# Kernel optimization log

Measured on AMD Instinct MI355X. Metric: run time of the kernel, lower is better.

The kernel has to match this reference:

```python
import jax, jax.numpy as jnp
import numpy as np

N = 100_000      # nodes
E = 3_200_000    # edges (avg degree 32)
D = 128          # input_dim == hidden_dim
L = 3            # num_layers
G = 64           # number of graphs in the batch
EPS = 1e-5       # LayerNorm eps


def setup_inputs() -> dict:
    key = jax.random.key(0)
    ks = jax.random.split(key, 8)
    x = jax.random.normal(ks[0], (N, D), dtype=jnp.float32)
    edge_index = jax.random.randint(ks[1], (2, E), 0, N, dtype=jnp.int64)
    edge_weight = jax.random.normal(ks[2], (E,), dtype=jnp.float32)
    batch = jnp.sort(jax.random.randint(ks[3], (N,), 0, G, dtype=jnp.int64))
    s = 1.0 / np.sqrt(D)
    W_pos = jax.random.normal(ks[4], (L, D, D), dtype=jnp.float32) * s
    W_neg = jax.random.normal(ks[5], (L, D, D), dtype=jnp.float32) * s
    b_pos = jnp.zeros((L, D), dtype=jnp.float32)
    b_neg = jnp.zeros((L, D), dtype=jnp.float32)
    gamma = jnp.ones((D,), dtype=jnp.float32)
    beta = jnp.zeros((D,), dtype=jnp.float32)
    return dict(x=x, edge_index=edge_index, edge_weight=edge_weight, batch=batch,
                W_pos=W_pos, b_pos=b_pos, W_neg=W_neg, b_neg=b_neg,
                gamma=gamma, beta=beta)


def _branch_norm(src, dst, mask, n):
    # GCN symmetric normalization on the masked subgraph with unit edge weights
    # and self-loops (fill_value=1). deg counted on target nodes (PyG col).
    deg = 1.0 + jax.ops.segment_sum(mask, dst, num_segments=n)  # >= 1
    dinv_sqrt = jax.lax.rsqrt(deg)
    edge_norm = mask * dinv_sqrt[src] * dinv_sqrt[dst]          # 0 on masked-out edges
    self_norm = 1.0 / deg                                       # self-loop coefficient
    return edge_norm, self_norm


def _gcn_layer(h, W, b, src, dst, edge_norm, self_norm):
    h = h @ W  # [N, H], lin without bias (PyG GCNConv)
    agg = jax.ops.segment_sum(edge_norm[:, None] * h[src], dst,
                              num_segments=h.shape[0])
    return agg + h * self_norm[:, None] + b


def reference(x, edge_index, edge_weight, batch, W_pos, b_pos, W_neg, b_neg, gamma, beta):
    src, dst = edge_index[0], edge_index[1]
    pos_mask = (edge_weight > 0).astype(x.dtype)
    neg_mask = (edge_weight < 0).astype(x.dtype)
    n = x.shape[0]
    pos_en, pos_sn = _branch_norm(src, dst, pos_mask, n)
    neg_en, neg_sn = _branch_norm(src, dst, neg_mask, n)
    h = x
    for l in range(W_pos.shape[0]):
        hp = _gcn_layer(h, W_pos[l], b_pos[l], src, dst, pos_en, pos_sn)
        hn = _gcn_layer(h, W_neg[l], b_neg[l], src, dst, neg_en, neg_sn)
        h = jax.nn.relu(hp) - jax.nn.relu(hn)
    # global mean pool over graphs
    counts = jax.ops.segment_sum(jnp.ones((n,), h.dtype), batch, num_segments=G)
    sums = jax.ops.segment_sum(h, batch, num_segments=G)
    pooled = sums / jnp.clip(counts, 1.0)[:, None]  # [G, H]
    # LayerNorm
    mu = jnp.mean(pooled, axis=-1, keepdims=True)
    var = jnp.mean(jnp.square(pooled - mu), axis=-1, keepdims=True)
    return (pooled - mu) * jax.lax.rsqrt(var + EPS) * gamma + beta
```

## Files before the change

kernel.cpp:

```cpp
#include <hip/hip_runtime.h>
#include <stdint.h>

typedef unsigned short u16;
typedef __attribute__((ext_vector_type(8))) short bfrag;
typedef __attribute__((ext_vector_type(4))) float f32x4;
typedef __attribute__((ext_vector_type(2))) float f32x2;

__device__ __forceinline__ uint32_t pack2bf(float x, float y) {
  uint32_t bx = __float_as_uint(x), by = __float_as_uint(y);
  bx += 0x7fffu + ((bx >> 16) & 1u);
  by += 0x7fffu + ((by >> 16) & 1u);
  return (bx >> 16) | (by & 0xffff0000u);
}
__device__ __forceinline__ u16 f2bf(float x) {
  uint32_t b = __float_as_uint(x);
  b += 0x7fffu + ((b >> 16) & 1u);
  return (u16)(b >> 16);
}
__device__ __forceinline__ float bflo(uint32_t p) { return __uint_as_float(p << 16); }
__device__ __forceinline__ float bfhi(uint32_t p) { return __uint_as_float(p & 0xffff0000u); }

__global__ void k_cvt_x(const float* __restrict__ x, uint32_t* __restrict__ xb, int n4) {
  int i = blockIdx.x * blockDim.x + threadIdx.x;
  if (i >= n4) return;
  float4 v = ((const float4*)x)[i];
  xb[2 * i]     = pack2bf(v.x, v.y);
  xb[2 * i + 1] = pack2bf(v.z, v.w);
}

__global__ void k_shadow(const uint32_t* __restrict__ xb, const float* __restrict__ dpn,
                         uint8_t* __restrict__ x8p, uint8_t* __restrict__ x8n, int n) {
  int gid = blockIdx.x * blockDim.x + threadIdx.x;
  int nd = gid >> 6, lane = gid & 63;
  if (nd >= n) return;
  float dp = dpn[2 * nd], dn = dpn[2 * nd + 1];
  uint32_t pk = xb[(size_t)nd * 64 + lane];
  float v0 = bflo(pk), v1 = bfhi(pk);
  *(u16*)(x8p + (size_t)nd * 128 + lane * 2) =
      (u16)(__builtin_amdgcn_cvt_pk_fp8_f32(dp * v0, dp * v1, 0u, false) & 0xffffu);
  *(u16*)(x8n + (size_t)nd * 128 + lane * 2) =
      (u16)(__builtin_amdgcn_cvt_pk_fp8_f32(dn * v0, dn * v1, 0u, false) & 0xffffu);
}

__global__ void k_cvt_w(const float* __restrict__ wp, const float* __restrict__ wn,
                        u16* __restrict__ wt, int total) {
  int i = blockIdx.x * blockDim.x + threadIdx.x;
  if (i >= total) return;
  int l = i >> 15;
  int rem = i & 32767;
  int br = rem >> 14;
  int rem2 = rem & 16383;
  int c = rem2 >> 7;
  int k = rem2 & 127;
  const float* w = br ? wn : wp;
  wt[i] = f2bf(w[l * 16384 + k * 128 + c]);
}

__global__ __launch_bounds__(256) void k_histA(
    const int* __restrict__ ei, const float* __restrict__ ew,
    int* __restrict__ histA, int E, int nbk, int nba) {
  __shared__ int h[1600];
  int blk = blockIdx.x, t = threadIdx.x;
  for (int b = t; b < nbk; b += 256) h[b] = 0;
  __syncthreads();
  int base = blk * 8192;
  int lim = base + 8192; if (lim > E) lim = E;
  for (int e = base + t; e < lim; e += 256) {
    if (ew[e] == 0.f) continue;
    atomicAdd(&h[ei[E + e] >> 6], 1);
  }
  __syncthreads();
  for (int b = t; b < nbk; b += 256) histA[(size_t)b * nba + blk] = h[b];
}

__global__ void k_scan1(const int* __restrict__ cnt, int* __restrict__ offs,
                        int* __restrict__ part, int M) {
  __shared__ int sh[1024];
  int t = threadIdx.x;
  int i = blockIdx.x * 1024 + t;
  int v = (i < M) ? cnt[i] : 0;
  sh[t] = v;
  __syncthreads();
  for (int off = 1; off < 1024; off <<= 1) {
    int add = (t >= off) ? sh[t - off] : 0;
    __syncthreads();
    sh[t] += add;
    __syncthreads();
  }
  if (i < M) offs[i] = sh[t] - v;
  if (t == 1023) part[blockIdx.x] = sh[1023];
}
__global__ void k_scan2(int* __restrict__ part, int* __restrict__ offs,
                        uint32_t* __restrict__ recF, int nb, int M) {
  __shared__ int sh[1024];
  int t = threadIdx.x;
  int v = (t < nb) ? part[t] : 0;
  sh[t] = v;
  __syncthreads();
  for (int off = 1; off < 1024; off <<= 1) {
    int add = (t >= off) ? sh[t - off] : 0;
    __syncthreads();
    sh[t] += add;
    __syncthreads();
  }
  if (t < nb) part[t] = sh[t] - v;
  if (t == 1023) {
    int run = sh[1023];
    offs[M] = run;
    for (int i = 0; i < 32; ++i) recF[run + i] = 0u;
  }
}

__global__ __launch_bounds__(256) void k_partB(
    const int* __restrict__ ei, const float* __restrict__ ew,
    const int* __restrict__ offsA, const int* __restrict__ partA,
    uint32_t* __restrict__ rec4, int E, int nbk, int nba) {
  __shared__ int curs[1600];
  int blk = blockIdx.x, t = threadIdx.x;
  for (int b = t; b < nbk; b += 256) {
    int idx = b * nba + blk;
    curs[b] = offsA[idx] + partA[idx >> 10];
  }
  __syncthreads();
  int base = blk * 8192;
  int lim = base + 8192; if (lim > E) lim = E;
  for (int e = base + t; e < lim; e += 256) {
    float w = ew[e];
    if (w == 0.f) continue;
    int s = ei[e], d = ei[E + e];
    int pos = atomicAdd(&curs[d >> 6], 1);
    rec4[pos] = (uint32_t)s | ((w < 0.f ? 1u : 0u) << 17) | ((uint32_t)(d & 63) << 18);
  }
}

__global__ __launch_bounds__(256) void k_sortC(
    const uint32_t* __restrict__ rec4, const int* __restrict__ offsA,
    const int* __restrict__ partA, uint32_t* __restrict__ recF,
    int* __restrict__ bnd2, float* __restrict__ dpn,
    int n, int nbk, int nba, int SM) {
  __shared__ uint32_t rin[3072];
  __shared__ uint32_t rout[3072];
  __shared__ int hist[128];
  __shared__ int curs[128];
  int b = blockIdx.x, t = threadIdx.x;
  int i0 = b * nba;
  int beg = offsA[i0] + partA[i0 >> 10];
  int end;
  if (b + 1 < nbk) {
    int i1 = (b + 1) * nba;
    end = offsA[i1] + partA[i1 >> 10];
  } else {
    end = offsA[SM];
  }
  int cnt = end - beg;
  if (cnt > 3072) cnt = 3072;
  for (int i = t; i < cnt; i += 256) rin[i] = rec4[beg + i];
  if (t < 128) hist[t] = 0;
  __syncthreads();
  for (int i = t; i < cnt; i += 256)
    atomicAdd(&hist[(rin[i] >> 17) & 127], 1);
  __syncthreads();
  if (t == 0) {
    int run = 0;
    for (int k = 0; k < 128; ++k) { int c = hist[k]; curs[k] = run; run += c; }
  }
  __syncthreads();
  if (t < 64) {
    int node = b * 64 + t;
    if (node < n) {
      bnd2[2 * node]     = beg + curs[t * 2];
      bnd2[2 * node + 1] = beg + curs[t * 2 + 1];
      int degp = hist[t * 2], degn = hist[t * 2 + 1];
      dpn[2 * node]     = rsqrtf(1.f + (float)degp);
      dpn[2 * node + 1] = rsqrtf(1.f + (float)degn);
    }
  }
  if (t == 0 && b == nbk - 1) bnd2[2 * n] = end;
  __syncthreads();
  for (int i = t; i < cnt; i += 256) {
    uint32_t r = rin[i];
    int pos = atomicAdd(&curs[(r >> 17) & 127], 1);
    rout[pos] = r & 0x1FFFFu;
  }
  __syncthreads();
  for (int i = t; i < cnt; i += 256) recF[beg + i] = rout[i];
}

__global__ __launch_bounds__(256) void k_agg(
    const uint32_t* __restrict__ hin,
    const uint8_t* __restrict__ x8p, const uint8_t* __restrict__ x8n,
    const int* __restrict__ bnd2, const uint32_t* __restrict__ rec,
    const float* __restrict__ dpn,
    uint32_t* __restrict__ up, uint32_t* __restrict__ un, int n) {
  int gid = blockIdx.x * blockDim.x + threadIdx.x;
  int nd = gid >> 6, lane = gid & 63;
  if (nd >= n) return;
  int beg = bnd2[2 * nd], mid = bnd2[2 * nd + 1], end = bnd2[2 * nd + 2];
  float ap0 = 0.f, ap1 = 0.f, an0 = 0.f, an1 = 0.f;
  for (int j = beg; j < mid; j += 8) {
    uint32_t rr[8]; u16 pk[8];
#pragma unroll
    for (int u = 0; u < 8; ++u) rr[u] = rec[j + u];
#pragma unroll
    for (int u = 0; u < 8; ++u)
      pk[u] = *(const u16*)(x8p + (size_t)rr[u] * 128 + lane * 2);
#pragma unroll
    for (int u = 0; u < 8; ++u) {
      u16 pm = (j + u < mid) ? pk[u] : (u16)0;
      f32x2 v = __builtin_amdgcn_cvt_pk_f32_fp8((uint32_t)pm, false);
      ap0 += v.x;
      ap1 += v.y;
    }
  }
  for (int j = mid; j < end; j += 8) {
    uint32_t rr[8]; u16 pk[8];
#pragma unroll
    for (int u = 0; u < 8; ++u) rr[u] = rec[j + u];
#pragma unroll
    for (int u = 0; u < 8; ++u)
      pk[u] = *(const u16*)(x8n + (size_t)rr[u] * 128 + lane * 2);
#pragma unroll
    for (int u = 0; u < 8; ++u) {
      u16 pm = (j + u < end) ? pk[u] : (u16)0;
      f32x2 v = __builtin_amdgcn_cvt_pk_f32_fp8((uint32_t)pm, false);
      an0 += v.x;
      an1 += v.y;
    }
  }
  float dpd = dpn[2 * nd], dnd = dpn[2 * nd + 1];
  float sp = dpd * dpd, sn = dnd * dnd;
  uint32_t hk = hin[(size_t)nd * 64 + lane];
  float h0 = bflo(hk), h1 = bfhi(hk);
  up[(size_t)nd * 64 + lane] = pack2bf(fmaf(sp, h0, dpd * ap0), fmaf(sp, h1, dpd * ap1));
  un[(size_t)nd * 64 + lane] = pack2bf(fmaf(sn, h0, dnd * an0), fmaf(sn, h1, dnd * an1));
}

__global__ __launch_bounds__(256, 2) void k_gemm(
    const short* __restrict__ up, const short* __restrict__ un,
    const u16* __restrict__ wt, const float* __restrict__ bp, const float* __restrict__ bn,
    const float* __restrict__ dpn,
    u16* __restrict__ hout, uint8_t* __restrict__ x8p, uint8_t* __restrict__ x8n,
    int nrows, int nchunks) {
  __shared__ __align__(16) u16 wl[32768];
  __shared__ __align__(16) u16 ct[4][8][132];
  __shared__ __align__(16) uint8_t ct8[4][8][144];
  int t = threadIdx.x;
  for (int i = t; i < 4096; i += 256) {
    int ci = i & 2047;
    int col = ci >> 4, kc16 = ci & 15;
    int db = (i >> 11) * 32768 + ((col * 256 + kc16 * 16) ^ ((col & 7) << 4));
    *(uint4*)((char*)wl + db) = ((const uint4*)wt)[i];
  }
  __syncthreads();
  int wv = t >> 6, lane = t & 63;
  int l15 = lane & 15, l4 = lane >> 4;
  float vbp[8], vbn[8];
#pragma unroll
  for (int nt = 0; nt < 8; ++nt) {
    vbp[nt] = bp[nt * 16 + l15];
    vbn[nt] = bn[nt * 16 + l15];
  }
  for (int c = blockIdx.x; c < nchunks; c += gridDim.x) {
    int rowbase = c * 128 + wv * 32;
    int r0 = rowbase + l15;      if (r0 >= nrows) r0 = nrows - 1;
    int r1 = rowbase + 16 + l15; if (r1 >= nrows) r1 = nrows - 1;
    f32x4 accP[2][8], accN[2][8];
#pragma unroll
    for (int rt = 0; rt < 2; ++rt)
#pragma unroll
      for (int nt = 0; nt < 8; ++nt) { accP[rt][nt] = (f32x4)(0.f); accN[rt][nt] = (f32x4)(0.f); }
#pragma unroll
    for (int kc = 0; kc < 4; ++kc) {
      int koff = kc * 32 + l4 * 8;
      bfrag aP0 = *(const bfrag*)(up + (size_t)r0 * 128 + koff);
      bfrag aP1 = *(const bfrag*)(up + (size_t)r1 * 128 + koff);
      bfrag aN0 = *(const bfrag*)(un + (size_t)r0 * 128 + koff);
      bfrag aN1 = *(const bfrag*)(un + (size_t)r1 * 128 + koff);
#pragma unroll
      for (int nt = 0; nt < 8; ++nt) {
        int col = nt * 16 + l15;
        int bb = (col * 256 + kc * 64 + l4 * 16) ^ ((col & 7) << 4);
        bfrag bP = *(const bfrag*)((const char*)wl + bb);
        bfrag bN = *(const bfrag*)((const char*)wl + 32768 + bb);
        accP[0][nt] = __builtin_amdgcn_mfma_f32_16x16x32_bf16(aP0, bP, accP[0][nt], 0, 0, 0);
        accP[1][nt] = __builtin_amdgcn_mfma_f32_16x16x32_bf16(aP1, bP, accP[1][nt], 0, 0, 0);
        accN[0][nt] = __builtin_amdgcn_mfma_f32_16x16x32_bf16(aN0, bN, accN[0][nt], 0, 0, 0);
        accN[1][nt] = __builtin_amdgcn_mfma_f32_16x16x32_bf16(aN1, bN, accN[1][nt], 0, 0, 0);
      }
    }
#pragma unroll
    for (int rt = 0; rt < 2; ++rt) {
#pragma unroll
      for (int h = 0; h < 2; ++h) {
        if ((l4 >> 1) == h) {
          int lr = (l4 & 1) * 4;
#pragma unroll
          for (int r = 0; r < 4; ++r) {
            int rw = rowbase + rt * 16 + h * 8 + lr + r;
            if (rw >= nrows) rw = nrows - 1;
            float dpr = dpn[2 * rw];
#pragma unroll
            for (int nt = 0; nt < 8; ++nt) {
              int col = nt * 16 + l15;
              float vp = accP[rt][nt][r] + vbp[nt]; vp = vp > 0.f ? vp : 0.f;
              float vn = accN[rt][nt][r] + vbn[nt]; vn = vn > 0.f ? vn : 0.f;
              float hv = vp - vn;
              ct[wv][lr + r][col] = f2bf(hv);
              ct8[wv][lr + r][col] =
                  (uint8_t)(__builtin_amdgcn_cvt_pk_fp8_f32(dpr * hv, dpr * hv, 0u, false) & 0xffu);
            }
          }
        }
#pragma unroll
        for (int i = 0; i < 2; ++i) {
          int lrow = i * 4 + (l4 & 3);
          int grow = rowbase + rt * 16 + h * 8 + lrow;
          uint4 vv = *(const uint4*)&ct[wv][lrow][l15 * 8];
          if (grow < nrows)
            *(uint4*)(hout + (size_t)grow * 128 + l15 * 8) = vv;
        }
        {
          int lrow = lane >> 3, lch = lane & 7;
          int grow = rowbase + rt * 16 + h * 8 + lrow;
          uint4 b16 = *(const uint4*)&ct8[wv][lrow][lch * 16];
          if (grow < nrows)
            *(uint4*)(x8p + (size_t)grow * 128 + lch * 16) = b16;
        }
        if ((l4 >> 1) == h) {
          int lr = (l4 & 1) * 4;
#pragma unroll
          for (int r = 0; r < 4; ++r) {
            int rw = rowbase + rt * 16 + h * 8 + lr + r;
            if (rw >= nrows) rw = nrows - 1;
            float dnr = dpn[2 * rw + 1];
#pragma unroll
            for (int nt = 0; nt < 8; ++nt) {
              int col = nt * 16 + l15;
              float vp = accP[rt][nt][r] + vbp[nt]; vp = vp > 0.f ? vp : 0.f;
              float vn = accN[rt][nt][r] + vbn[nt]; vn = vn > 0.f ? vn : 0.f;
              float hv = vp - vn;
              ct8[wv][lr + r][col] =
                  (uint8_t)(__builtin_amdgcn_cvt_pk_fp8_f32(dnr * hv, dnr * hv, 0u, false) & 0xffu);
            }
          }
        }
        {
          int lrow = lane >> 3, lch = lane & 7;
          int grow = rowbase + rt * 16 + h * 8 + lrow;
          uint4 b16 = *(const uint4*)&ct8[wv][lrow][lch * 16];
          if (grow < nrows)
            *(uint4*)(x8n + (size_t)grow * 128 + lch * 16) = b16;
        }
      }
    }
  }
}

__global__ void k_pool(const uint32_t* __restrict__ h, const int* __restrict__ batch,
                       float* __restrict__ pooled, float* __restrict__ gcnt, int n) {
  int gid = blockIdx.x * blockDim.x + threadIdx.x;
  int w = gid >> 6, lane = gid & 63;
  int n0 = w * 8;
  if (n0 >= n) return;
  int curg = -1, c = 0;
  float a0 = 0.f, a1 = 0.f;
  for (int i = 0; i < 8; ++i) {
    int nd = n0 + i;
    if (nd >= n) break;
    int g = batch[nd];
    if (g != curg) {
      if (curg >= 0) {
        atomicAdd(&pooled[curg * 128 + 2 * lane], a0);
        atomicAdd(&pooled[curg * 128 + 2 * lane + 1], a1);
        if (lane == 0) atomicAdd(gcnt + curg, (float)c);
      }
      curg = g; a0 = a1 = 0.f; c = 0;
    }
    uint32_t pk = h[(size_t)nd * 64 + lane];
    a0 += bflo(pk); a1 += bfhi(pk); ++c;
  }
  if (curg >= 0) {
    atomicAdd(&pooled[curg * 128 + 2 * lane], a0);
    atomicAdd(&pooled[curg * 128 + 2 * lane + 1], a1);
    if (lane == 0) atomicAdd(gcnt + curg, (float)c);
  }
}

__global__ void k_ln(const float* __restrict__ pooled, const float* __restrict__ gcnt,
                     const float* __restrict__ gamma, const float* __restrict__ beta,
                     float* __restrict__ out, int G) {
  int gid = blockIdx.x * blockDim.x + threadIdx.x;
  int g = gid >> 6, lane = gid & 63;
  if (g >= G) return;
  float2 s = ((const float2*)pooled)[g * 64 + lane];
  float cm = fmaxf(gcnt[g], 1.f);
  float v0 = s.x / cm, v1 = s.y / cm;
  float tsum = v0 + v1;
#pragma unroll
  for (int m = 1; m < 64; m <<= 1) tsum += __shfl_xor(tsum, m, 64);
  float mu = tsum * (1.f / 128.f);
  float d0 = v0 - mu, d1 = v1 - mu;
  float q = d0 * d0 + d1 * d1;
#pragma unroll
  for (int m = 1; m < 64; m <<= 1) q += __shfl_xor(q, m, 64);
  float inv = rsqrtf(q * (1.f / 128.f) + 1e-5f);
  int f = 2 * lane;
  out[g * 128 + f]     = d0 * inv * gamma[f]     + beta[f];
  out[g * 128 + f + 1] = d1 * inv * gamma[f + 1] + beta[f + 1];
}

extern "C" void kernel_launch(void* const* d_in, const int* in_sizes, int n_in,
                              void* d_out, int out_size, void* d_ws, size_t ws_size,
                              hipStream_t stream) {
  const float* x     = (const float*)d_in[0];
  const int* ei      = (const int*)d_in[1];
  const float* ew    = (const float*)d_in[2];
  const int* bt      = (const int*)d_in[3];
  const float* Wp    = (const float*)d_in[4];
  const float* bp    = (const float*)d_in[5];
  const float* Wn    = (const float*)d_in[6];
  const float* bn    = (const float*)d_in[7];
  const float* gamma = (const float*)d_in[8];
  const float* beta  = (const float*)d_in[9];
  int N = in_sizes[0] / 128;
  int E = in_sizes[1] / 2;
  int L = in_sizes[4] / (128 * 128);
  int G = out_size / 128;
  int nbk = (N + 63) / 64;
  int nba = (E + 8191) / 8192;
  int SM = nbk * nba;

  char* w = (char*)d_ws;
  auto alloc = [&](size_t bytes) {
    char* p = w;
    w += (bytes + 255) & ~(size_t)255;
    return p;
  };
  uint32_t* X    = (uint32_t*)alloc((size_t)N * 128 * 2);
  uint8_t* X8p   = (uint8_t*)alloc((size_t)N * 128 + 256);
  uint8_t* X8n   = (uint8_t*)alloc((size_t)N * 128 + 256);
  uint32_t* U    = (uint32_t*)alloc((size_t)N * 128 * 2);
  uint32_t* V    = (uint32_t*)alloc((size_t)N * 128 * 2);
  u16* wt        = (u16*)alloc((size_t)L * 2 * 128 * 128 * 2);
  uint32_t* rec4 = (uint32_t*)alloc(((size_t)E + 32) * 4);
  uint32_t* recF = (uint32_t*)alloc(((size_t)E + 32) * 4);
  int* histA     = (int*)alloc((size_t)SM * 4);
  int* offsA     = (int*)alloc((size_t)(SM + 1) * 4);
  int* partA     = (int*)alloc(1024 * 4);
  int* bnd2      = (int*)alloc((size_t)(2 * N + 1) * 4);
  float* dpn     = (float*)alloc((size_t)N * 8);
  float* pooled  = (float*)alloc((size_t)G * 128 * 4);
  float* gcnt    = (float*)alloc((size_t)G * 4);

  hipMemsetAsync(pooled, 0, (size_t)G * 128 * 4, stream);
  hipMemsetAsync(gcnt, 0, (size_t)G * 4, stream);

  int n4 = N * 32;
  int wtot = L * 2 * 128 * 128;
  k_cvt_x<<<(n4 + 255) / 256, 256, 0, stream>>>(x, X, n4);
  k_cvt_w<<<(wtot + 255) / 256, 256, 0, stream>>>(Wp, Wn, wt, wtot);
  k_histA<<<nba, 256, 0, stream>>>(ei, ew, histA, E, nbk, nba);
  int NB1 = (SM + 1023) / 1024;
  k_scan1<<<NB1, 1024, 0, stream>>>(histA, offsA, partA, SM);
  k_scan2<<<1, 1024, 0, stream>>>(partA, offsA, recF, NB1, SM);
  k_partB<<<nba, 256, 0, stream>>>(ei, ew, offsA, partA, rec4, E, nbk, nba);
  k_sortC<<<nbk, 256, 0, stream>>>(rec4, offsA, partA, recF, bnd2, dpn, N, nbk, nba, SM);
  k_shadow<<<((size_t)N * 64 + 255) / 256, 256, 0, stream>>>(X, dpn, X8p, X8n, N);

  int nchunks = (N + 127) / 128;
  for (int l = 0; l < L; ++l) {
    k_agg<<<((size_t)N * 64 + 255) / 256, 256, 0, stream>>>(X, X8p, X8n, bnd2, recF, dpn, U, V, N);
    k_gemm<<<512, 256, 0, stream>>>((const short*)U, (const short*)V,
                                    wt + (size_t)l * 32768, bp + (size_t)l * 128,
                                    bn + (size_t)l * 128, dpn, (u16*)X, X8p, X8n, N, nchunks);
  }
  k_pool<<<(((N + 7) / 8) * 64 + 255) / 256, 256, 0, stream>>>(X, bt, pooled, gcnt, N);
  k_ln<<<(G * 64 + 255) / 256, 256, 0, stream>>>(pooled, gcnt, gamma, beta, (float*)d_out, G);
}
```

Measured before the change: 632.2 us.

## Fuse mean pooling into last-layer GEMM epilogue and derive graph counts by binary search

On the final layer, the GEMM epilogue no longer writes h (bf16 and fp8 shadows). It reduces the activated rows per graph straight from the MFMA accumulators, using LDS and global atomics, and the separate pooling kernel is removed. Node counts per graph now come from a binary search over the sorted batch array in the LayerNorm kernel, which drops the count atomics and one memset. This saves a full read of the hidden state and the last layer's stores, at the cost of extra barriers and atomics inside the GEMM. Pooling now sums fp32 values rather than bf16-rounded ones.

```diff
diff --git a/kernel.cpp b/kernel.cpp
--- a/kernel.cpp
+++ b/kernel.cpp
@@ -238,12 +238,13 @@
 __global__ __launch_bounds__(256, 2) void k_gemm(
     const short* __restrict__ up, const short* __restrict__ un,
     const u16* __restrict__ wt, const float* __restrict__ bp, const float* __restrict__ bn,
-    const float* __restrict__ dpn,
+    const float* __restrict__ dpn, const int* __restrict__ batch,
     u16* __restrict__ hout, uint8_t* __restrict__ x8p, uint8_t* __restrict__ x8n,
-    int nrows, int nchunks) {
+    float* __restrict__ pooled, int do_pool, int nrows, int nchunks) {
   __shared__ __align__(16) u16 wl[32768];
   __shared__ __align__(16) u16 ct[4][8][132];
   __shared__ __align__(16) uint8_t ct8[4][8][144];
+  __shared__ float pacc[128];
   int t = threadIdx.x;
   for (int i = t; i < 4096; i += 256) {
     int ci = i & 2047;
@@ -288,6 +289,58 @@
         accN[1][nt] = __builtin_amdgcn_mfma_f32_16x16x32_bf16(aN1, bN, accN[1][nt], 0, 0, 0);
       }
     }
+    if (do_pool) {
+      int crow0 = c * 128;
+      int crow1 = crow0 + 127; if (crow1 >= nrows) crow1 = nrows - 1;
+      int g0 = batch[crow0], g1 = batch[crow1];
+      if (t < 128) pacc[t] = 0.f;
+      __syncthreads();
+      if (g0 == g1) {
+#pragma unroll
+        for (int nt = 0; nt < 8; ++nt) {
+          float s = 0.f;
+#pragma unroll
+          for (int rt = 0; rt < 2; ++rt) {
+#pragma unroll
+            for (int r = 0; r < 4; ++r) {
+              int row = rowbase + rt * 16 + l4 * 4 + r;
+              float vp = accP[rt][nt][r] + vbp[nt]; vp = vp > 0.f ? vp : 0.f;
+              float vn = accN[rt][nt][r] + vbn[nt]; vn = vn > 0.f ? vn : 0.f;
+              s += (row < nrows) ? (vp - vn) : 0.f;
+            }
+          }
+          s += __shfl_xor(s, 16, 64);
+          s += __shfl_xor(s, 32, 64);
+          if (l4 == 0) atomicAdd(&pacc[nt * 16 + l15], s);
+        }
+        __syncthreads();
+        if (t < 128) atomicAdd(&pooled[g0 * 128 + t], pacc[t]);
+      } else {
+        for (int g = g0; g <= g1; ++g) {
+#pragma unroll
+          for (int nt = 0; nt < 8; ++nt) {
+            float s = 0.f;
+#pragma unroll
+            for (int rt = 0; rt < 2; ++rt) {
+#pragma unroll
+              for (int r = 0; r < 4; ++r) {
+                int row = rowbase + rt * 16 + l4 * 4 + r;
+                bool in = (row < nrows) && (batch[row] == g);
+                float vp = accP[rt][nt][r] + vbp[nt]; vp = vp > 0.f ? vp : 0.f;
+                float vn = accN[rt][nt][r] + vbn[nt]; vn = vn > 0.f ? vn : 0.f;
+                s += in ? (vp - vn) : 0.f;
+              }
+            }
+            s += __shfl_xor(s, 16, 64);
+            s += __shfl_xor(s, 32, 64);
+            if (l4 == 0) atomicAdd(&pooled[g * 128 + nt * 16 + l15], s);
+          }
+        }
+        __syncthreads();
+      }
+      __syncthreads();
+      continue;
+    }
 #pragma unroll
     for (int rt = 0; rt < 2; ++rt) {
 #pragma unroll
@@ -356,44 +409,20 @@
   }
 }
 
-__global__ void k_pool(const uint32_t* __restrict__ h, const int* __restrict__ batch,
-                       float* __restrict__ pooled, float* __restrict__ gcnt, int n) {
-  int gid = blockIdx.x * blockDim.x + threadIdx.x;
-  int w = gid >> 6, lane = gid & 63;
-  int n0 = w * 8;
-  if (n0 >= n) return;
-  int curg = -1, c = 0;
-  float a0 = 0.f, a1 = 0.f;
-  for (int i = 0; i < 8; ++i) {
-    int nd = n0 + i;
-    if (nd >= n) break;
-    int g = batch[nd];
-    if (g != curg) {
-      if (curg >= 0) {
-        atomicAdd(&pooled[curg * 128 + 2 * lane], a0);
-        atomicAdd(&pooled[curg * 128 + 2 * lane + 1], a1);
-        if (lane == 0) atomicAdd(gcnt + curg, (float)c);
-      }
-      curg = g; a0 = a1 = 0.f; c = 0;
-    }
-    uint32_t pk = h[(size_t)nd * 64 + lane];
-    a0 += bflo(pk); a1 += bfhi(pk); ++c;
-  }
-  if (curg >= 0) {
-    atomicAdd(&pooled[curg * 128 + 2 * lane], a0);
-    atomicAdd(&pooled[curg * 128 + 2 * lane + 1], a1);
-    if (lane == 0) atomicAdd(gcnt + curg, (float)c);
-  }
-}
-
-__global__ void k_ln(const float* __restrict__ pooled, const float* __restrict__ gcnt,
+__global__ void k_ln(const float* __restrict__ pooled, const int* __restrict__ batch,
                      const float* __restrict__ gamma, const float* __restrict__ beta,
-                     float* __restrict__ out, int G) {
+                     float* __restrict__ out, int G, int n) {
   int gid = blockIdx.x * blockDim.x + threadIdx.x;
   int g = gid >> 6, lane = gid & 63;
   if (g >= G) return;
+  int lo = 0, hi = n;
+  while (lo < hi) { int m = (lo + hi) >> 1; if (batch[m] < g) lo = m + 1; else hi = m; }
+  int s0 = lo;
+  lo = s0; hi = n;
+  while (lo < hi) { int m = (lo + hi) >> 1; if (batch[m] < g + 1) lo = m + 1; else hi = m; }
+  int e0 = lo;
   float2 s = ((const float2*)pooled)[g * 64 + lane];
-  float cm = fmaxf(gcnt[g], 1.f);
+  float cm = fmaxf((float)(e0 - s0), 1.f);
   float v0 = s.x / cm, v1 = s.y / cm;
   float tsum = v0 + v1;
 #pragma unroll
@@ -450,10 +479,8 @@
   int* bnd2      = (int*)alloc((size_t)(2 * N + 1) * 4);
   float* dpn     = (float*)alloc((size_t)N * 8);
   float* pooled  = (float*)alloc((size_t)G * 128 * 4);
-  float* gcnt    = (float*)alloc((size_t)G * 4);
 
   hipMemsetAsync(pooled, 0, (size_t)G * 128 * 4, stream);
-  hipMemsetAsync(gcnt, 0, (size_t)G * 4, stream);
 
   int n4 = N * 32;
   int wtot = L * 2 * 128 * 128;
@@ -472,8 +499,9 @@
     k_agg<<<((size_t)N * 64 + 255) / 256, 256, 0, stream>>>(X, X8p, X8n, bnd2, recF, dpn, U, V, N);
     k_gemm<<<512, 256, 0, stream>>>((const short*)U, (const short*)V,
                                     wt + (size_t)l * 32768, bp + (size_t)l * 128,
-                                    bn + (size_t)l * 128, dpn, (u16*)X, X8p, X8n, N, nchunks);
-  }
-  k_pool<<<(((N + 7) / 8) * 64 + 255) / 256, 256, 0, stream>>>(X, bt, pooled, gcnt, N);
-  k_ln<<<(G * 64 + 255) / 256, 256, 0, stream>>>(pooled, gcnt, gamma, beta, (float*)d_out, G);
-}
+                                    bn + (size_t)l * 128, dpn, bt,
+                                    (u16*)X, X8p, X8n, pooled, (l == L - 1) ? 1 : 0,
+                                    N, nchunks);
+  }
+  k_ln<<<(G * 64 + 255) / 256, 256, 0, stream>>>(pooled, bt, gamma, beta, (float*)d_out, G, N);
+}
```

Measured after the change: 596.1 us. 5.7% less time.
